# Kernel tuning notes

Hardware: AMD Instinct MI355X
Metric: run time of the kernel (lower is better)

## Reference

```python
import jax, jax.numpy as jnp
import numpy as np

N = 100000
E = 1600000
F_IN = 128
HID = 64
HID2 = 32
NCLS = 2
EPS = 1e-5  # BatchNorm eps


def setup_inputs() -> dict:
    key = jax.random.key(0)
    ks = jax.random.split(key, 12)
    inp = {
        'x': jax.random.normal(ks[0], (N, F_IN), dtype=jnp.float32),
        'edge_index': jax.random.randint(ks[1], (2, E), 0, N, dtype=jnp.int64),
        # GCNConv layer 1: weight [F_IN, HID], bias [HID]
        'W1': jax.random.normal(ks[2], (F_IN, HID), dtype=jnp.float32) / np.sqrt(F_IN),
        'b1': jnp.zeros((HID,), dtype=jnp.float32),
        # GCNConv layer 2
        'W2': jax.random.normal(ks[3], (HID, HID2), dtype=jnp.float32) / np.sqrt(HID),
        'b2': jnp.zeros((HID2,), dtype=jnp.float32),
        # BatchNorm1d params (eval mode: running stats)
        'g1': jax.random.uniform(ks[4], (HID,), dtype=jnp.float32, minval=0.5, maxval=1.5),
        'be1': jax.random.normal(ks[5], (HID,), dtype=jnp.float32) * 0.1,
        'rm1': jax.random.normal(ks[6], (HID,), dtype=jnp.float32) * 0.1,
        'rv1': jax.random.uniform(ks[7], (HID,), dtype=jnp.float32, minval=0.5, maxval=1.5),
        'g2': jax.random.uniform(ks[8], (HID2,), dtype=jnp.float32, minval=0.5, maxval=1.5),
        'be2': jax.random.normal(ks[9], (HID2,), dtype=jnp.float32) * 0.1,
        'rm2': jax.random.normal(ks[10], (HID2,), dtype=jnp.float32) * 0.1,
        'rv2': jax.random.uniform(ks[11], (HID2,), dtype=jnp.float32, minval=0.5, maxval=1.5),
        # classifier
        'Wc': jax.random.normal(jax.random.fold_in(key, 99), (HID2, NCLS), dtype=jnp.float32) / np.sqrt(HID2),
        'bc': jnp.zeros((NCLS,), dtype=jnp.float32),
    }
    return inp


def _gcn_conv(x, src, dst, norm, W, b, n_nodes):
    # PyG GCNConv: transform -> gather source -> norm-weight -> scatter-add -> +bias
    h = x @ W                                  # [N, out]
    msg = h[src] * norm[:, None]               # [E+N, out] gathered messages
    out = jax.ops.segment_sum(msg, dst, num_segments=n_nodes)
    return out + b


def _bn_eval(x, gamma, beta, rmean, rvar):
    return (x - rmean) * (gamma * jax.lax.rsqrt(rvar + EPS)) + beta


def reference(x, edge_index, W1, b1, W2, b2, g1, be1, rm1, rv1, g2, be2, rm2, rv2, Wc, bc):
    n = x.shape[0]
    loop = jnp.arange(n, dtype=edge_index.dtype)
    src = jnp.concatenate([edge_index[0], loop])   # add self-loops
    dst = jnp.concatenate([edge_index[1], loop])
    # symmetric degree normalization on A + I (degree counted at target)
    deg = jax.ops.segment_sum(jnp.ones_like(dst, dtype=x.dtype), dst, num_segments=n)
    dinv = jnp.where(deg > 0, jax.lax.rsqrt(deg), 0.0)
    norm = dinv[src] * dinv[dst]                   # [E+N]

    h = _gcn_conv(x, src, dst, norm, W1, b1, n)
    h = jax.nn.relu(_bn_eval(h, g1, be1, rm1, rv1))
    # dropout: identity in eval mode
    h = _gcn_conv(h, src, dst, norm, W2, b2, n)
    h = jax.nn.relu(_bn_eval(h, g2, be2, rm2, rv2))
    logits = h @ Wc + bc
    return jax.nn.log_softmax(logits, axis=1)
```

## Files before the change

### kernel.cpp

```cpp
#include <hip/hip_runtime.h>
#include <hip/hip_fp16.h>
#include <math.h>

#define F_IN 128
#define HID 64
#define HID2 32
#define EPS_BN 1e-5f
#define BW 128
#define NBMAX 1024
#define CAP 2560
#define CH 8192

__global__ __launch_bounds__(256) void partition_kernel(const int* __restrict__ src, const int* __restrict__ dst,
                                                        int E, int* __restrict__ gcursor,
                                                        unsigned* __restrict__ ebuf) {
    __shared__ int hist[NBMAX];
    __shared__ int start[NBMAX];
    __shared__ int cur[NBMAX];
    __shared__ int gb[NBMAX];
    __shared__ int stmp[256];
    __shared__ unsigned buf[CH];
    int tid = threadIdx.x;
    int e0 = blockIdx.x * CH;
#pragma unroll
    for (int i = 0; i < NBMAX / 256; i++) hist[tid + 256 * i] = 0;
    __syncthreads();
    for (int k = tid; k < CH; k += 256) {
        int e = e0 + k;
        if (e < E) atomicAdd(&hist[dst[e] >> 7], 1);
    }
    __syncthreads();
    int s0 = hist[4 * tid], s1 = hist[4 * tid + 1], s2 = hist[4 * tid + 2], s3 = hist[4 * tid + 3];
    int tsum = s0 + s1 + s2 + s3;
    stmp[tid] = tsum;
    __syncthreads();
    for (int off = 1; off < 256; off <<= 1) {
        int t = (tid >= off) ? stmp[tid - off] : 0;
        __syncthreads();
        stmp[tid] += t;
        __syncthreads();
    }
    int ex = stmp[tid] - tsum;
    start[4 * tid + 0] = ex;                cur[4 * tid + 0] = ex;
    start[4 * tid + 1] = ex + s0;           cur[4 * tid + 1] = ex + s0;
    start[4 * tid + 2] = ex + s0 + s1;      cur[4 * tid + 2] = ex + s0 + s1;
    start[4 * tid + 3] = ex + s0 + s1 + s2; cur[4 * tid + 3] = ex + s0 + s1 + s2;
#pragma unroll
    for (int j = 0; j < 4; j++) {
        int b = 4 * tid + j;
        int h = hist[b];
        gb[b] = h ? atomicAdd(&gcursor[b], h) : 0;
    }
    __syncthreads();
    for (int k = tid; k < CH; k += 256) {
        int e = e0 + k;
        if (e < E) {
            int d = dst[e], s = src[e];
            int p = atomicAdd(&cur[d >> 7], 1);
            buf[p] = ((unsigned)(d & (BW - 1)) << 17) | (unsigned)s;
        }
    }
    __syncthreads();
    int grp = tid >> 2, sub = tid & 3;
    for (int b = grp; b < NBMAX; b += 64) {
        int len = hist[b];
        if (!len) continue;
        int st = start[b];
        unsigned* dp = ebuf + (size_t)b * CAP + gb[b];
        for (int i = sub; i < len; i += 4) dp[i] = buf[st + i];
    }
}

__global__ __launch_bounds__(256) void localsort_kernel(unsigned* __restrict__ ebuf, const int* __restrict__ gcursor,
                                                        int* __restrict__ ns, int* __restrict__ ne,
                                                        float* __restrict__ dinv, int n) {
    __shared__ unsigned lbuf[CAP];
    __shared__ int lhist[BW];
    __shared__ int lcur[BW];
    __shared__ int stmp[256];
    int b = blockIdx.x;
    int tid = threadIdx.x;
    int base = b * CAP;
    int len = gcursor[b];
    int node0 = b * BW;
    int nn = min(BW, n - node0);
    if (tid < BW) lhist[tid] = 0;
    __syncthreads();
    for (int k = tid; k < len; k += 256) {
        unsigned u = ebuf[base + k];
        lbuf[k] = u;
        atomicAdd(&lhist[u >> 17], 1);
    }
    __syncthreads();
    int v = (tid < BW) ? lhist[tid] : 0;
    stmp[tid] = v;
    __syncthreads();
    for (int off = 1; off < 256; off <<= 1) {
        int t = (tid >= off) ? stmp[tid - off] : 0;
        __syncthreads();
        stmp[tid] += t;
        __syncthreads();
    }
    int ex = stmp[tid] - v;
    if (tid < BW) lcur[tid] = ex;
    if (tid < nn) {
        ns[node0 + tid] = base + ex;
        ne[node0 + tid] = base + ex + v;
        dinv[node0 + tid] = rsqrtf((float)(v + 1));
    }
    __syncthreads();
    for (int k = tid; k < len; k += 256) {
        unsigned u = lbuf[k];
        int p = atomicAdd(&lcur[u >> 17], 1);
        ebuf[base + p] = u & 0x1FFFFu;
    }
}

__global__ void constprep_kernel(const float* g1, const float* be1, const float* rm1, const float* rv1, const float* b1,
                                 const float* g2, const float* be2, const float* rm2, const float* rv2, const float* b2,
                                 float* A1, float* B1, float* A2, float* B2) {
    int t = threadIdx.x;
    if (t < HID)  { float s = g1[t] * rsqrtf(rv1[t] + EPS_BN); A1[t] = s; B1[t] = (b1[t] - rm1[t]) * s + be1[t]; }
    if (t < HID2) { float s = g2[t] * rsqrtf(rv2[t] + EPS_BN); A2[t] = s; B2[t] = (b2[t] - rm2[t]) * s + be2[t]; }
}

#define XP1 132
__global__ __launch_bounds__(256) void gemm1_kernel(const float* __restrict__ x, const float* __restrict__ W1,
                                                    const float* __restrict__ dinv, __half* __restrict__ ht1,
                                                    int n) {
    __shared__ float wlds[F_IN * HID];
    __shared__ float xlds[64 * XP1];
    int tid = threadIdx.x;
    {
        const float4* wv = (const float4*)W1;
        float4* wl = (float4*)wlds;
#pragma unroll
        for (int i = 0; i < F_IN * HID / 4 / 256; i++) wl[tid + 256 * i] = wv[tid + 256 * i];
    }
    int row0 = blockIdx.x * 64;
    {
        const float4* xv = (const float4*)(x + (size_t)row0 * F_IN);
        int lim = (n - row0) * (F_IN / 4);
#pragma unroll
        for (int i = 0; i < 8; i++) {
            int f = tid + 256 * i;
            float4 v = make_float4(0.f, 0.f, 0.f, 0.f);
            if (f < lim) v = xv[f];
            int r = f >> 5, kp = (f & 31) * 4;
            *(float4*)&xlds[r * XP1 + kp] = v;
        }
    }
    __syncthreads();
    int col4 = (tid & 15) * 4;
    int rowg = tid >> 4;
    float acc[4][4];
#pragma unroll
    for (int r = 0; r < 4; r++)
#pragma unroll
        for (int c = 0; c < 4; c++) acc[r][c] = 0.f;
#pragma unroll 4
    for (int k = 0; k < F_IN; k += 4) {
        float4 wb[4];
#pragma unroll
        for (int j = 0; j < 4; j++) wb[j] = *(const float4*)&wlds[(k + j) * HID + col4];
#pragma unroll
        for (int r = 0; r < 4; r++) {
            float4 xa = *(const float4*)&xlds[(rowg * 4 + r) * XP1 + k];
            acc[r][0] = fmaf(xa.x, wb[0].x, acc[r][0]); acc[r][1] = fmaf(xa.x, wb[0].y, acc[r][1]);
            acc[r][2] = fmaf(xa.x, wb[0].z, acc[r][2]); acc[r][3] = fmaf(xa.x, wb[0].w, acc[r][3]);
            acc[r][0] = fmaf(xa.y, wb[1].x, acc[r][0]); acc[r][1] = fmaf(xa.y, wb[1].y, acc[r][1]);
            acc[r][2] = fmaf(xa.y, wb[1].z, acc[r][2]); acc[r][3] = fmaf(xa.y, wb[1].w, acc[r][3]);
            acc[r][0] = fmaf(xa.z, wb[2].x, acc[r][0]); acc[r][1] = fmaf(xa.z, wb[2].y, acc[r][1]);
            acc[r][2] = fmaf(xa.z, wb[2].z, acc[r][2]); acc[r][3] = fmaf(xa.z, wb[2].w, acc[r][3]);
            acc[r][0] = fmaf(xa.w, wb[3].x, acc[r][0]); acc[r][1] = fmaf(xa.w, wb[3].y, acc[r][1]);
            acc[r][2] = fmaf(xa.w, wb[3].z, acc[r][2]); acc[r][3] = fmaf(xa.w, wb[3].w, acc[r][3]);
        }
    }
    int rbase = row0 + rowg * 4;
#pragma unroll
    for (int r = 0; r < 4; r++) {
        int row = rbase + r;
        if (row < n) {
            float d = dinv[row];
            __half2 h0, h1;
            h0.x = __float2half(acc[r][0] * d); h0.y = __float2half(acc[r][1] * d);
            h1.x = __float2half(acc[r][2] * d); h1.y = __float2half(acc[r][3] * d);
            __half2* dp = (__half2*)(ht1 + (size_t)row * HID + col4);
            dp[0] = h0; dp[1] = h1;
        }
    }
}

#define XP2 68
__global__ __launch_bounds__(256) void gemm2_kernel(const float* __restrict__ h1p, const float* __restrict__ W2,
                                                    const float* __restrict__ dinv, __half* __restrict__ ht2,
                                                    int n) {
    __shared__ float wlds[HID * HID2];
    __shared__ float xlds[64 * XP2];
    int tid = threadIdx.x;
    {
        const float4* wv = (const float4*)W2;
        float4* wl = (float4*)wlds;
#pragma unroll
        for (int i = 0; i < HID * HID2 / 4 / 256; i++) wl[tid + 256 * i] = wv[tid + 256 * i];
    }
    int row0 = blockIdx.x * 64;
    {
        const float4* xv = (const float4*)(h1p + (size_t)row0 * HID);
        int lim = (n - row0) * (HID / 4);
#pragma unroll
        for (int i = 0; i < 4; i++) {
            int f = tid + 256 * i;
            float4 v = make_float4(0.f, 0.f, 0.f, 0.f);
            if (f < lim) v = xv[f];
            int r = f >> 4, kp = (f & 15) * 4;
            *(float4*)&xlds[r * XP2 + kp] = v;
        }
    }
    __syncthreads();
    int col4 = (tid & 7) * 4;
    int rowg = tid >> 3;
    float acc[2][4];
#pragma unroll
    for (int r = 0; r < 2; r++)
#pragma unroll
        for (int c = 0; c < 4; c++) acc[r][c] = 0.f;
#pragma unroll 4
    for (int k = 0; k < HID; k += 4) {
        float4 wb[4];
#pragma unroll
        for (int j = 0; j < 4; j++) wb[j] = *(const float4*)&wlds[(k + j) * HID2 + col4];
#pragma unroll
        for (int r = 0; r < 2; r++) {
            float4 xa = *(const float4*)&xlds[(rowg * 2 + r) * XP2 + k];
            acc[r][0] = fmaf(xa.x, wb[0].x, acc[r][0]); acc[r][1] = fmaf(xa.x, wb[0].y, acc[r][1]);
            acc[r][2] = fmaf(xa.x, wb[0].z, acc[r][2]); acc[r][3] = fmaf(xa.x, wb[0].w, acc[r][3]);
            acc[r][0] = fmaf(xa.y, wb[1].x, acc[r][0]); acc[r][1] = fmaf(xa.y, wb[1].y, acc[r][1]);
            acc[r][2] = fmaf(xa.y, wb[1].z, acc[r][2]); acc[r][3] = fmaf(xa.y, wb[1].w, acc[r][3]);
            acc[r][0] = fmaf(xa.z, wb[2].x, acc[r][0]); acc[r][1] = fmaf(xa.z, wb[2].y, acc[r][1]);
            acc[r][2] = fmaf(xa.z, wb[2].z, acc[r][2]); acc[r][3] = fmaf(xa.z, wb[2].w, acc[r][3]);
            acc[r][0] = fmaf(xa.w, wb[3].x, acc[r][0]); acc[r][1] = fmaf(xa.w, wb[3].y, acc[r][1]);
            acc[r][2] = fmaf(xa.w, wb[3].z, acc[r][2]); acc[r][3] = fmaf(xa.w, wb[3].w, acc[r][3]);
        }
    }
    int rbase = row0 + rowg * 2;
#pragma unroll
    for (int r = 0; r < 2; r++) {
        int row = rbase + r;
        if (row < n) {
            float d = dinv[row];
            __half2 h0, h1;
            h0.x = __float2half(acc[r][0] * d); h0.y = __float2half(acc[r][1] * d);
            h1.x = __float2half(acc[r][2] * d); h1.y = __float2half(acc[r][3] * d);
            __half2* dp = (__half2*)(ht2 + (size_t)row * HID2 + col4);
            dp[0] = h0; dp[1] = h1;
        }
    }
}

__global__ __launch_bounds__(256) void agg1_kernel(const __half* __restrict__ ht1, const int* __restrict__ ns,
                                                   const int* __restrict__ ne, const int* __restrict__ csr,
                                                   const float* __restrict__ dinv,
                                                   const float* __restrict__ A1, const float* __restrict__ B1,
                                                   float* __restrict__ h1p, int n) {
    int node = (blockIdx.x * blockDim.x + threadIdx.x) >> 6;
    node = __builtin_amdgcn_readfirstlane(node);
    int lane = threadIdx.x & 63;
    if (node >= n) return;
    int s = ns[node], e_end = ne[node];
    float acc = __half2float(ht1[(size_t)node * HID + lane]);
    int e = s;
    for (; e + 8 <= e_end; e += 8) {
        int i0 = csr[e + 0], i1 = csr[e + 1], i2 = csr[e + 2], i3 = csr[e + 3];
        int i4 = csr[e + 4], i5 = csr[e + 5], i6 = csr[e + 6], i7 = csr[e + 7];
        float v0 = __half2float(ht1[(size_t)i0 * HID + lane]);
        float v1 = __half2float(ht1[(size_t)i1 * HID + lane]);
        float v2 = __half2float(ht1[(size_t)i2 * HID + lane]);
        float v3 = __half2float(ht1[(size_t)i3 * HID + lane]);
        float v4 = __half2float(ht1[(size_t)i4 * HID + lane]);
        float v5 = __half2float(ht1[(size_t)i5 * HID + lane]);
        float v6 = __half2float(ht1[(size_t)i6 * HID + lane]);
        float v7 = __half2float(ht1[(size_t)i7 * HID + lane]);
        acc += ((v0 + v1) + (v2 + v3)) + ((v4 + v5) + (v6 + v7));
    }
    for (; e + 4 <= e_end; e += 4) {
        int i0 = csr[e + 0], i1 = csr[e + 1], i2 = csr[e + 2], i3 = csr[e + 3];
        float v0 = __half2float(ht1[(size_t)i0 * HID + lane]);
        float v1 = __half2float(ht1[(size_t)i1 * HID + lane]);
        float v2 = __half2float(ht1[(size_t)i2 * HID + lane]);
        float v3 = __half2float(ht1[(size_t)i3 * HID + lane]);
        acc += (v0 + v1) + (v2 + v3);
    }
    for (; e < e_end; e++) acc += __half2float(ht1[(size_t)csr[e] * HID + lane]);
    float v = acc * dinv[node];
    v = fmaxf(fmaf(v, A1[lane], B1[lane]), 0.f);
    h1p[(size_t)node * HID + lane] = v;
}

__global__ __launch_bounds__(256) void agg2_kernel(const __half* __restrict__ ht2, const int* __restrict__ ns,
                                                   const int* __restrict__ ne, const int* __restrict__ csr,
                                                   const float* __restrict__ dinv,
                                                   const float* __restrict__ A2, const float* __restrict__ B2,
                                                   const float* __restrict__ Wc, const float* __restrict__ bc,
                                                   float* __restrict__ out, int n) {
    int node = (blockIdx.x * blockDim.x + threadIdx.x) >> 6;
    node = __builtin_amdgcn_readfirstlane(node);
    int lane = threadIdx.x & 63;
    if (node >= n) return;
    int c = lane & 31, p = lane >> 5;
    int s = ns[node], e_end = ne[node];
    float acc = (p == 0) ? __half2float(ht2[(size_t)node * HID2 + c]) : 0.f;
    int e = s + p;
    for (; e + 6 < e_end; e += 8) {
        int i0 = csr[e + 0], i1 = csr[e + 2], i2 = csr[e + 4], i3 = csr[e + 6];
        float v0 = __half2float(ht2[(size_t)i0 * HID2 + c]);
        float v1 = __half2float(ht2[(size_t)i1 * HID2 + c]);
        float v2 = __half2float(ht2[(size_t)i2 * HID2 + c]);
        float v3 = __half2float(ht2[(size_t)i3 * HID2 + c]);
        acc += (v0 + v1) + (v2 + v3);
    }
    for (; e < e_end; e += 2) acc += __half2float(ht2[(size_t)csr[e] * HID2 + c]);
    acc += __shfl_xor(acc, 32);
    float v = fmaxf(fmaf(acc * dinv[node], A2[c], B2[c]), 0.f);
    float p0 = v * Wc[c * 2 + 0];
    float p1 = v * Wc[c * 2 + 1];
#pragma unroll
    for (int off = 16; off >= 1; off >>= 1) { p0 += __shfl_xor(p0, off); p1 += __shfl_xor(p1, off); }
    if (lane == 0) {
        float l0 = p0 + bc[0], l1 = p1 + bc[1];
        float m = fmaxf(l0, l1);
        float lse = m + logf(expf(l0 - m) + expf(l1 - m));
        out[(size_t)node * 2 + 0] = l0 - lse;
        out[(size_t)node * 2 + 1] = l1 - lse;
    }
}

extern "C" void kernel_launch(void* const* d_in, const int* in_sizes, int n_in,
                              void* d_out, int out_size, void* d_ws, size_t ws_size,
                              hipStream_t stream) {
    const float* x   = (const float*)d_in[0];
    const int*   ei  = (const int*)d_in[1];
    const float* W1  = (const float*)d_in[2];
    const float* b1  = (const float*)d_in[3];
    const float* W2  = (const float*)d_in[4];
    const float* b2  = (const float*)d_in[5];
    const float* g1  = (const float*)d_in[6];
    const float* be1 = (const float*)d_in[7];
    const float* rm1 = (const float*)d_in[8];
    const float* rv1 = (const float*)d_in[9];
    const float* g2  = (const float*)d_in[10];
    const float* be2 = (const float*)d_in[11];
    const float* rm2 = (const float*)d_in[12];
    const float* rv2 = (const float*)d_in[13];
    const float* Wc  = (const float*)d_in[14];
    const float* bc  = (const float*)d_in[15];
    float* out = (float*)d_out;

    int n = in_sizes[0] / F_IN;
    int E = in_sizes[1] / 2;
    const int* srcv = ei;
    const int* dstv = ei + E;
    int NB = (n + BW - 1) / BW;

    char* ws = (char*)d_ws;
    size_t off = 0;
    auto alloc = [&](size_t bytes) -> char* {
        char* r = ws + off;
        off = (off + bytes + 511) & ~(size_t)511;
        return r;
    };
    int*      gcursor = (int*)alloc((size_t)NB * 4);
    int*      ns      = (int*)alloc((size_t)n * 4);
    int*      ne      = (int*)alloc((size_t)n * 4);
    float*    dinv    = (float*)alloc((size_t)n * 4);
    float*    A1 = (float*)alloc(HID * 4);
    float*    B1 = (float*)alloc(HID * 4);
    float*    A2 = (float*)alloc(HID2 * 4);
    float*    B2 = (float*)alloc(HID2 * 4);
    unsigned* ebuf = (unsigned*)alloc((size_t)NB * CAP * 4);
    __half*   ht1  = (__half*)alloc((size_t)n * HID * 2);
    float*    h1p  = (float*)alloc((size_t)n * HID * 4);
    __half*   ht2  = ht1;

    hipMemsetAsync(gcursor, 0, (size_t)NB * 4, stream);

    int nch = (E + CH - 1) / CH;
    partition_kernel<<<nch, 256, 0, stream>>>(srcv, dstv, E, gcursor, ebuf);
    localsort_kernel<<<NB, 256, 0, stream>>>(ebuf, gcursor, ns, ne, dinv, n);
    constprep_kernel<<<1, 64, 0, stream>>>(g1, be1, rm1, rv1, b1, g2, be2, rm2, rv2, b2, A1, B1, A2, B2);

    int ngb = (n + 63) / 64;
    gemm1_kernel<<<ngb, 256, 0, stream>>>(x, W1, dinv, ht1, n);
    agg1_kernel<<<(n + 3) / 4, 256, 0, stream>>>(ht1, ns, ne, (const int*)ebuf, dinv, A1, B1, h1p, n);
    gemm2_kernel<<<ngb, 256, 0, stream>>>(h1p, W2, dinv, ht2, n);
    agg2_kernel<<<(n + 3) / 4, 256, 0, stream>>>(ht2, ns, ne, (const int*)ebuf, dinv, A2, B2, Wc, bc, out, n);
}
```

Baseline: 310.3 us.

## Replace per-node CSR sort with bucket-level LDS atomic aggregation

Drops the local sort, so edges stay bucketed by 128-node destination block with packed local ids. The aggregation kernels now run one block per bucket and accumulate gathered half-precision features into padded shared-memory tiles with LDS float atomics, then apply BN/ReLU (and the classifier) from shared memory. The partition kernel moves to 1024 threads with one histogram bin per thread, and a small degree kernel replaces localsort for dinv. This removes a full pass over the edge buffer, but float LDS atomics can contend and make summation order nondeterministic, and only NB (~782) blocks run per aggregation.

After: 1.200 ms. 3.87x slower.

```diff
diff --git a/kernel.cpp b/kernel.cpp
--- a/kernel.cpp
+++ b/kernel.cpp
@@ -11,49 +11,42 @@
 #define CAP 2560
 #define CH 8192
 
-__global__ __launch_bounds__(256) void partition_kernel(const int* __restrict__ src, const int* __restrict__ dst,
-                                                        int E, int* __restrict__ gcursor,
-                                                        unsigned* __restrict__ ebuf) {
+__global__ __launch_bounds__(1024) void partition_kernel(const int* __restrict__ src, const int* __restrict__ dst,
+                                                         int E, int* __restrict__ gcursor,
+                                                         unsigned* __restrict__ ebuf) {
     __shared__ int hist[NBMAX];
     __shared__ int start[NBMAX];
     __shared__ int cur[NBMAX];
     __shared__ int gb[NBMAX];
-    __shared__ int stmp[256];
+    __shared__ int sc[1024];
     __shared__ unsigned buf[CH];
     int tid = threadIdx.x;
     int e0 = blockIdx.x * CH;
-#pragma unroll
-    for (int i = 0; i < NBMAX / 256; i++) hist[tid + 256 * i] = 0;
-    __syncthreads();
-    for (int k = tid; k < CH; k += 256) {
-        int e = e0 + k;
+    hist[tid] = 0;
+    __syncthreads();
+#pragma unroll
+    for (int it = 0; it < CH / 1024; it++) {
+        int e = e0 + tid + it * 1024;
         if (e < E) atomicAdd(&hist[dst[e] >> 7], 1);
     }
     __syncthreads();
-    int s0 = hist[4 * tid], s1 = hist[4 * tid + 1], s2 = hist[4 * tid + 2], s3 = hist[4 * tid + 3];
-    int tsum = s0 + s1 + s2 + s3;
-    stmp[tid] = tsum;
-    __syncthreads();
-    for (int off = 1; off < 256; off <<= 1) {
-        int t = (tid >= off) ? stmp[tid - off] : 0;
+    int v = hist[tid];
+    sc[tid] = v;
+    __syncthreads();
+    for (int off = 1; off < 1024; off <<= 1) {
+        int t = (tid >= off) ? sc[tid - off] : 0;
         __syncthreads();
-        stmp[tid] += t;
+        sc[tid] += t;
         __syncthreads();
     }
-    int ex = stmp[tid] - tsum;
-    start[4 * tid + 0] = ex;                cur[4 * tid + 0] = ex;
-    start[4 * tid + 1] = ex + s0;           cur[4 * tid + 1] = ex + s0;
-    start[4 * tid + 2] = ex + s0 + s1;      cur[4 * tid + 2] = ex + s0 + s1;
-    start[4 * tid + 3] = ex + s0 + s1 + s2; cur[4 * tid + 3] = ex + s0 + s1 + s2;
-#pragma unroll
-    for (int j = 0; j < 4; j++) {
-        int b = 4 * tid + j;
-        int h = hist[b];
-        gb[b] = h ? atomicAdd(&gcursor[b], h) : 0;
-    }
-    __syncthreads();
-    for (int k = tid; k < CH; k += 256) {
-        int e = e0 + k;
+    int ex = sc[tid] - v;
+    start[tid] = ex;
+    cur[tid] = ex;
+    gb[tid] = v ? atomicAdd(&gcursor[tid], v) : 0;
+    __syncthreads();
+#pragma unroll
+    for (int it = 0; it < CH / 1024; it++) {
+        int e = e0 + tid + it * 1024;
         if (e < E) {
             int d = dst[e], s = src[e];
             int p = atomicAdd(&cur[d >> 7], 1);
@@ -62,7 +55,7 @@
     }
     __syncthreads();
     int grp = tid >> 2, sub = tid & 3;
-    for (int b = grp; b < NBMAX; b += 64) {
+    for (int b = grp; b < NBMAX; b += 256) {
         int len = hist[b];
         if (!len) continue;
         int st = start[b];
@@ -71,49 +64,18 @@
     }
 }
 
-__global__ __launch_bounds__(256) void localsort_kernel(unsigned* __restrict__ ebuf, const int* __restrict__ gcursor,
-                                                        int* __restrict__ ns, int* __restrict__ ne,
-                                                        float* __restrict__ dinv, int n) {
-    __shared__ unsigned lbuf[CAP];
-    __shared__ int lhist[BW];
-    __shared__ int lcur[BW];
-    __shared__ int stmp[256];
-    int b = blockIdx.x;
-    int tid = threadIdx.x;
-    int base = b * CAP;
-    int len = gcursor[b];
+__global__ __launch_bounds__(256) void degree_kernel(const unsigned* __restrict__ ebuf, const int* __restrict__ gcursor,
+                                                     float* __restrict__ dinv, int n) {
+    __shared__ int ldeg[BW];
+    int b = blockIdx.x, tid = threadIdx.x;
+    int base = b * CAP, len = gcursor[b];
     int node0 = b * BW;
     int nn = min(BW, n - node0);
-    if (tid < BW) lhist[tid] = 0;
-    __syncthreads();
-    for (int k = tid; k < len; k += 256) {
-        unsigned u = ebuf[base + k];
-        lbuf[k] = u;
-        atomicAdd(&lhist[u >> 17], 1);
-    }
-    __syncthreads();
-    int v = (tid < BW) ? lhist[tid] : 0;
-    stmp[tid] = v;
-    __syncthreads();
-    for (int off = 1; off < 256; off <<= 1) {
-        int t = (tid >= off) ? stmp[tid - off] : 0;
-        __syncthreads();
-        stmp[tid] += t;
-        __syncthreads();
-    }
-    int ex = stmp[tid] - v;
-    if (tid < BW) lcur[tid] = ex;
-    if (tid < nn) {
-        ns[node0 + tid] = base + ex;
-        ne[node0 + tid] = base + ex + v;
-        dinv[node0 + tid] = rsqrtf((float)(v + 1));
-    }
-    __syncthreads();
-    for (int k = tid; k < len; k += 256) {
-        unsigned u = lbuf[k];
-        int p = atomicAdd(&lcur[u >> 17], 1);
-        ebuf[base + p] = u & 0x1FFFFu;
-    }
+    if (tid < BW) ldeg[tid] = 0;
+    __syncthreads();
+    for (int k = tid; k < len; k += 256) atomicAdd(&ldeg[ebuf[base + k] >> 17], 1);
+    __syncthreads();
+    if (tid < nn) dinv[node0 + tid] = rsqrtf((float)(ldeg[tid] + 1));
 }
 
 __global__ void constprep_kernel(const float* g1, const float* be1, const float* rm1, const float* rv1, const float* b1,
@@ -258,80 +220,133 @@
     }
 }
 
-__global__ __launch_bounds__(256) void agg1_kernel(const __half* __restrict__ ht1, const int* __restrict__ ns,
-                                                   const int* __restrict__ ne, const int* __restrict__ csr,
-                                                   const float* __restrict__ dinv,
+#define FS1 65
+__global__ __launch_bounds__(256) void agg1_kernel(const __half* __restrict__ ht1, const unsigned* __restrict__ ebuf,
+                                                   const int* __restrict__ gcursor, const float* __restrict__ dinv,
                                                    const float* __restrict__ A1, const float* __restrict__ B1,
                                                    float* __restrict__ h1p, int n) {
-    int node = (blockIdx.x * blockDim.x + threadIdx.x) >> 6;
-    node = __builtin_amdgcn_readfirstlane(node);
-    int lane = threadIdx.x & 63;
-    if (node >= n) return;
-    int s = ns[node], e_end = ne[node];
-    float acc = __half2float(ht1[(size_t)node * HID + lane]);
-    int e = s;
-    for (; e + 8 <= e_end; e += 8) {
-        int i0 = csr[e + 0], i1 = csr[e + 1], i2 = csr[e + 2], i3 = csr[e + 3];
-        int i4 = csr[e + 4], i5 = csr[e + 5], i6 = csr[e + 6], i7 = csr[e + 7];
-        float v0 = __half2float(ht1[(size_t)i0 * HID + lane]);
-        float v1 = __half2float(ht1[(size_t)i1 * HID + lane]);
-        float v2 = __half2float(ht1[(size_t)i2 * HID + lane]);
-        float v3 = __half2float(ht1[(size_t)i3 * HID + lane]);
-        float v4 = __half2float(ht1[(size_t)i4 * HID + lane]);
-        float v5 = __half2float(ht1[(size_t)i5 * HID + lane]);
-        float v6 = __half2float(ht1[(size_t)i6 * HID + lane]);
-        float v7 = __half2float(ht1[(size_t)i7 * HID + lane]);
-        acc += ((v0 + v1) + (v2 + v3)) + ((v4 + v5) + (v6 + v7));
-    }
-    for (; e + 4 <= e_end; e += 4) {
-        int i0 = csr[e + 0], i1 = csr[e + 1], i2 = csr[e + 2], i3 = csr[e + 3];
-        float v0 = __half2float(ht1[(size_t)i0 * HID + lane]);
-        float v1 = __half2float(ht1[(size_t)i1 * HID + lane]);
-        float v2 = __half2float(ht1[(size_t)i2 * HID + lane]);
-        float v3 = __half2float(ht1[(size_t)i3 * HID + lane]);
-        acc += (v0 + v1) + (v2 + v3);
-    }
-    for (; e < e_end; e++) acc += __half2float(ht1[(size_t)csr[e] * HID + lane]);
-    float v = acc * dinv[node];
-    v = fmaxf(fmaf(v, A1[lane], B1[lane]), 0.f);
-    h1p[(size_t)node * HID + lane] = v;
-}
-
-__global__ __launch_bounds__(256) void agg2_kernel(const __half* __restrict__ ht2, const int* __restrict__ ns,
-                                                   const int* __restrict__ ne, const int* __restrict__ csr,
-                                                   const float* __restrict__ dinv,
+    __shared__ float facc[BW * FS1];
+    __shared__ float sA[HID], sB[HID];
+    __shared__ float ldinv[BW];
+    int b = blockIdx.x, tid = threadIdx.x;
+    int base = b * CAP, len = gcursor[b];
+    int node0 = b * BW;
+    int nn = min(BW, n - node0);
+    if (tid < HID) { sA[tid] = A1[tid]; sB[tid] = B1[tid]; }
+    if (tid < nn) ldinv[tid] = dinv[node0 + tid];
+    const __half2* htp = (const __half2*)ht1;
+    for (int idx = tid; idx < nn * 32; idx += 256) {
+        int row = idx >> 5, cp = idx & 31;
+        float2 f = __half22float2(htp[(size_t)(node0 + row) * 32 + cp]);
+        facc[row * FS1 + cp * 2] = f.x;
+        facc[row * FS1 + cp * 2 + 1] = f.y;
+    }
+    __syncthreads();
+    int wid = tid >> 6, lane = tid & 63;
+    int eh = lane >> 5;
+    int cp = lane & 31;
+    int col2 = cp * 2;
+    const unsigned* eb = ebuf + base;
+    int i = wid * 2 + eh;
+    for (; i + 24 < len; i += 32) {
+        unsigned u0 = eb[i], u1 = eb[i + 8], u2 = eb[i + 16], u3 = eb[i + 24];
+        float2 f0 = __half22float2(htp[(size_t)(u0 & 0x1FFFFu) * 32 + cp]);
+        float2 f1 = __half22float2(htp[(size_t)(u1 & 0x1FFFFu) * 32 + cp]);
+        float2 f2 = __half22float2(htp[(size_t)(u2 & 0x1FFFFu) * 32 + cp]);
+        float2 f3 = __half22float2(htp[(size_t)(u3 & 0x1FFFFu) * 32 + cp]);
+        atomicAdd(&facc[(u0 >> 17) * FS1 + col2], f0.x);
+        atomicAdd(&facc[(u0 >> 17) * FS1 + col2 + 1], f0.y);
+        atomicAdd(&facc[(u1 >> 17) * FS1 + col2], f1.x);
+        atomicAdd(&facc[(u1 >> 17) * FS1 + col2 + 1], f1.y);
+        atomicAdd(&facc[(u2 >> 17) * FS1 + col2], f2.x);
+        atomicAdd(&facc[(u2 >> 17) * FS1 + col2 + 1], f2.y);
+        atomicAdd(&facc[(u3 >> 17) * FS1 + col2], f3.x);
+        atomicAdd(&facc[(u3 >> 17) * FS1 + col2 + 1], f3.y);
+    }
+    for (; i < len; i += 8) {
+        unsigned u = eb[i];
+        float2 f = __half22float2(htp[(size_t)(u & 0x1FFFFu) * 32 + cp]);
+        atomicAdd(&facc[(u >> 17) * FS1 + col2], f.x);
+        atomicAdd(&facc[(u >> 17) * FS1 + col2 + 1], f.y);
+    }
+    __syncthreads();
+    for (int idx = tid; idx < nn * 32; idx += 256) {
+        int row = idx >> 5, cc = (idx & 31) * 2;
+        float d = ldinv[row];
+        float2 fr = *(float2*)&facc[row * FS1 + cc];
+        float2 o;
+        o.x = fmaxf(fmaf(fr.x * d, sA[cc], sB[cc]), 0.f);
+        o.y = fmaxf(fmaf(fr.y * d, sA[cc + 1], sB[cc + 1]), 0.f);
+        *(float2*)&h1p[(size_t)(node0 + row) * HID + cc] = o;
+    }
+}
+
+#define FS2 33
+__global__ __launch_bounds__(256) void agg2_kernel(const __half* __restrict__ ht2, const unsigned* __restrict__ ebuf,
+                                                   const int* __restrict__ gcursor, const float* __restrict__ dinv,
                                                    const float* __restrict__ A2, const float* __restrict__ B2,
                                                    const float* __restrict__ Wc, const float* __restrict__ bc,
                                                    float* __restrict__ out, int n) {
-    int node = (blockIdx.x * blockDim.x + threadIdx.x) >> 6;
-    node = __builtin_amdgcn_readfirstlane(node);
-    int lane = threadIdx.x & 63;
-    if (node >= n) return;
-    int c = lane & 31, p = lane >> 5;
-    int s = ns[node], e_end = ne[node];
-    float acc = (p == 0) ? __half2float(ht2[(size_t)node * HID2 + c]) : 0.f;
-    int e = s + p;
-    for (; e + 6 < e_end; e += 8) {
-        int i0 = csr[e + 0], i1 = csr[e + 2], i2 = csr[e + 4], i3 = csr[e + 6];
-        float v0 = __half2float(ht2[(size_t)i0 * HID2 + c]);
-        float v1 = __half2float(ht2[(size_t)i1 * HID2 + c]);
-        float v2 = __half2float(ht2[(size_t)i2 * HID2 + c]);
-        float v3 = __half2float(ht2[(size_t)i3 * HID2 + c]);
-        acc += (v0 + v1) + (v2 + v3);
-    }
-    for (; e < e_end; e += 2) acc += __half2float(ht2[(size_t)csr[e] * HID2 + c]);
-    acc += __shfl_xor(acc, 32);
-    float v = fmaxf(fmaf(acc * dinv[node], A2[c], B2[c]), 0.f);
-    float p0 = v * Wc[c * 2 + 0];
-    float p1 = v * Wc[c * 2 + 1];
-#pragma unroll
-    for (int off = 16; off >= 1; off >>= 1) { p0 += __shfl_xor(p0, off); p1 += __shfl_xor(p1, off); }
-    if (lane == 0) {
+    __shared__ float facc[BW * FS2];
+    __shared__ float sA[HID2], sB[HID2], sW[HID2 * 2];
+    __shared__ float ldinv[BW];
+    int b = blockIdx.x, tid = threadIdx.x;
+    int base = b * CAP, len = gcursor[b];
+    int node0 = b * BW;
+    int nn = min(BW, n - node0);
+    if (tid < HID2) { sA[tid] = A2[tid]; sB[tid] = B2[tid]; }
+    if (tid >= 64 && tid < 64 + HID2 * 2) sW[tid - 64] = Wc[tid - 64];
+    if (tid < nn) ldinv[tid] = dinv[node0 + tid];
+    const __half2* htp = (const __half2*)ht2;
+    for (int idx = tid; idx < nn * 16; idx += 256) {
+        int row = idx >> 4, cp = idx & 15;
+        float2 f = __half22float2(htp[(size_t)(node0 + row) * 16 + cp]);
+        facc[row * FS2 + cp * 2] = f.x;
+        facc[row * FS2 + cp * 2 + 1] = f.y;
+    }
+    __syncthreads();
+    int wid = tid >> 6, lane = tid & 63;
+    int eq = lane >> 4;
+    int cp = lane & 15;
+    int col2 = cp * 2;
+    const unsigned* eb = ebuf + base;
+    int i = wid * 4 + eq;
+    for (; i + 48 < len; i += 64) {
+        unsigned u0 = eb[i], u1 = eb[i + 16], u2 = eb[i + 32], u3 = eb[i + 48];
+        float2 f0 = __half22float2(htp[(size_t)(u0 & 0x1FFFFu) * 16 + cp]);
+        float2 f1 = __half22float2(htp[(size_t)(u1 & 0x1FFFFu) * 16 + cp]);
+        float2 f2 = __half22float2(htp[(size_t)(u2 & 0x1FFFFu) * 16 + cp]);
+        float2 f3 = __half22float2(htp[(size_t)(u3 & 0x1FFFFu) * 16 + cp]);
+        atomicAdd(&facc[(u0 >> 17) * FS2 + col2], f0.x);
+        atomicAdd(&facc[(u0 >> 17) * FS2 + col2 + 1], f0.y);
+        atomicAdd(&facc[(u1 >> 17) * FS2 + col2], f1.x);
+        atomicAdd(&facc[(u1 >> 17) * FS2 + col2 + 1], f1.y);
+        atomicAdd(&facc[(u2 >> 17) * FS2 + col2], f2.x);
+        atomicAdd(&facc[(u2 >> 17) * FS2 + col2 + 1], f2.y);
+        atomicAdd(&facc[(u3 >> 17) * FS2 + col2], f3.x);
+        atomicAdd(&facc[(u3 >> 17) * FS2 + col2 + 1], f3.y);
+    }
+    for (; i < len; i += 16) {
+        unsigned u = eb[i];
+        float2 f = __half22float2(htp[(size_t)(u & 0x1FFFFu) * 16 + cp]);
+        atomicAdd(&facc[(u >> 17) * FS2 + col2], f.x);
+        atomicAdd(&facc[(u >> 17) * FS2 + col2 + 1], f.y);
+    }
+    __syncthreads();
+    if (tid < nn) {
+        float d = ldinv[tid];
+        float p0 = 0.f, p1 = 0.f;
+#pragma unroll
+        for (int c = 0; c < HID2; c++) {
+            float v = fmaxf(fmaf(facc[tid * FS2 + c] * d, sA[c], sB[c]), 0.f);
+            p0 = fmaf(v, sW[c * 2 + 0], p0);
+            p1 = fmaf(v, sW[c * 2 + 1], p1);
+        }
         float l0 = p0 + bc[0], l1 = p1 + bc[1];
         float m = fmaxf(l0, l1);
         float lse = m + logf(expf(l0 - m) + expf(l1 - m));
-        out[(size_t)node * 2 + 0] = l0 - lse;
-        out[(size_t)node * 2 + 1] = l1 - lse;
+        float2 o; o.x = l0 - lse; o.y = l1 - lse;
+        *(float2*)&out[(size_t)(node0 + tid) * 2] = o;
     }
 }
 
@@ -370,8 +385,6 @@
         return r;
     };
     int*      gcursor = (int*)alloc((size_t)NB * 4);
-    int*      ns      = (int*)alloc((size_t)n * 4);
-    int*      ne      = (int*)alloc((size_t)n * 4);
     float*    dinv    = (float*)alloc((size_t)n * 4);
     float*    A1 = (float*)alloc(HID * 4);
     float*    B1 = (float*)alloc(HID * 4);
@@ -385,13 +398,13 @@
     hipMemsetAsync(gcursor, 0, (size_t)NB * 4, stream);
 
     int nch = (E + CH - 1) / CH;
-    partition_kernel<<<nch, 256, 0, stream>>>(srcv, dstv, E, gcursor, ebuf);
-    localsort_kernel<<<NB, 256, 0, stream>>>(ebuf, gcursor, ns, ne, dinv, n);
+    partition_kernel<<<nch, 1024, 0, stream>>>(srcv, dstv, E, gcursor, ebuf);
+    degree_kernel<<<NB, 256, 0, stream>>>(ebuf, gcursor, dinv, n);
     constprep_kernel<<<1, 64, 0, stream>>>(g1, be1, rm1, rv1, b1, g2, be2, rm2, rv2, b2, A1, B1, A2, B2);
 
     int ngb = (n + 63) / 64;
     gemm1_kernel<<<ngb, 256, 0, stream>>>(x, W1, dinv, ht1, n);
-    agg1_kernel<<<(n + 3) / 4, 256, 0, stream>>>(ht1, ns, ne, (const int*)ebuf, dinv, A1, B1, h1p, n);
+    agg1_kernel<<<NB, 256, 0, stream>>>(ht1, ebuf, gcursor, dinv, A1, B1, h1p, n);
     gemm2_kernel<<<ngb, 256, 0, stream>>>(h1p, W2, dinv, ht2, n);
-    agg2_kernel<<<(n + 3) / 4, 256, 0, stream>>>(ht2, ns, ne, (const int*)ebuf, dinv, A2, B2, Wc, bc, out, n);
-}
+    agg2_kernel<<<NB, 256, 0, stream>>>(ht2, ebuf, gcursor, dinv, A2, B2, Wc, bc, out, n);
+}
```

## Widen partition blocks and split neighbor lists across half-wave groups in aggregation

Applied to the files above, without the earlier changes.

The partition kernel now runs 1024 threads per block, one histogram bin per thread, with a single-bin scan and a wider copy-out loop. Both aggregation kernels now read features as half2, so 32 (agg1) or 16 (agg2) lanes cover a row. The remaining lanes split the neighbor list into 2 or 4 interleaved edge streams, which are combined with cross-lane shuffles. This is meant to raise memory-level parallelism and use wider loads in the gather-bound aggregation. The cost is extra shuffles and a longer 1024-wide scan with more barriers in partition.

Result: faster. 301.3 us (-2.9%).

```diff
diff --git a/kernel.cpp b/kernel.cpp
--- a/kernel.cpp
+++ b/kernel.cpp
@@ -11,49 +11,42 @@
 #define CAP 2560
 #define CH 8192
 
-__global__ __launch_bounds__(256) void partition_kernel(const int* __restrict__ src, const int* __restrict__ dst,
-                                                        int E, int* __restrict__ gcursor,
-                                                        unsigned* __restrict__ ebuf) {
+__global__ __launch_bounds__(1024) void partition_kernel(const int* __restrict__ src, const int* __restrict__ dst,
+                                                         int E, int* __restrict__ gcursor,
+                                                         unsigned* __restrict__ ebuf) {
     __shared__ int hist[NBMAX];
     __shared__ int start[NBMAX];
     __shared__ int cur[NBMAX];
     __shared__ int gb[NBMAX];
-    __shared__ int stmp[256];
+    __shared__ int sc[1024];
     __shared__ unsigned buf[CH];
     int tid = threadIdx.x;
     int e0 = blockIdx.x * CH;
-#pragma unroll
-    for (int i = 0; i < NBMAX / 256; i++) hist[tid + 256 * i] = 0;
-    __syncthreads();
-    for (int k = tid; k < CH; k += 256) {
-        int e = e0 + k;
+    hist[tid] = 0;
+    __syncthreads();
+#pragma unroll
+    for (int it = 0; it < CH / 1024; it++) {
+        int e = e0 + tid + it * 1024;
         if (e < E) atomicAdd(&hist[dst[e] >> 7], 1);
     }
     __syncthreads();
-    int s0 = hist[4 * tid], s1 = hist[4 * tid + 1], s2 = hist[4 * tid + 2], s3 = hist[4 * tid + 3];
-    int tsum = s0 + s1 + s2 + s3;
-    stmp[tid] = tsum;
-    __syncthreads();
-    for (int off = 1; off < 256; off <<= 1) {
-        int t = (tid >= off) ? stmp[tid - off] : 0;
+    int v = hist[tid];
+    sc[tid] = v;
+    __syncthreads();
+    for (int off = 1; off < 1024; off <<= 1) {
+        int t = (tid >= off) ? sc[tid - off] : 0;
         __syncthreads();
-        stmp[tid] += t;
+        sc[tid] += t;
         __syncthreads();
     }
-    int ex = stmp[tid] - tsum;
-    start[4 * tid + 0] = ex;                cur[4 * tid + 0] = ex;
-    start[4 * tid + 1] = ex + s0;           cur[4 * tid + 1] = ex + s0;
-    start[4 * tid + 2] = ex + s0 + s1;      cur[4 * tid + 2] = ex + s0 + s1;
-    start[4 * tid + 3] = ex + s0 + s1 + s2; cur[4 * tid + 3] = ex + s0 + s1 + s2;
-#pragma unroll
-    for (int j = 0; j < 4; j++) {
-        int b = 4 * tid + j;
-        int h = hist[b];
-        gb[b] = h ? atomicAdd(&gcursor[b], h) : 0;
-    }
-    __syncthreads();
-    for (int k = tid; k < CH; k += 256) {
-        int e = e0 + k;
+    int ex = sc[tid] - v;
+    start[tid] = ex;
+    cur[tid] = ex;
+    gb[tid] = v ? atomicAdd(&gcursor[tid], v) : 0;
+    __syncthreads();
+#pragma unroll
+    for (int it = 0; it < CH / 1024; it++) {
+        int e = e0 + tid + it * 1024;
         if (e < E) {
             int d = dst[e], s = src[e];
             int p = atomicAdd(&cur[d >> 7], 1);
@@ -62,7 +55,7 @@
     }
     __syncthreads();
     int grp = tid >> 2, sub = tid & 3;
-    for (int b = grp; b < NBMAX; b += 64) {
+    for (int b = grp; b < NBMAX; b += 256) {
         int len = hist[b];
         if (!len) continue;
         int st = start[b];
@@ -264,37 +257,45 @@
                                                    const float* __restrict__ A1, const float* __restrict__ B1,
                                                    float* __restrict__ h1p, int n) {
     int node = (blockIdx.x * blockDim.x + threadIdx.x) >> 6;
-    node = __builtin_amdgcn_readfirstlane(node);
+    if (node >= n) return;
     int lane = threadIdx.x & 63;
-    if (node >= n) return;
+    int eh = lane >> 5, cp = lane & 31;
+    const __half2* htp = (const __half2*)ht1;
     int s = ns[node], e_end = ne[node];
-    float acc = __half2float(ht1[(size_t)node * HID + lane]);
-    int e = s;
-    for (; e + 8 <= e_end; e += 8) {
-        int i0 = csr[e + 0], i1 = csr[e + 1], i2 = csr[e + 2], i3 = csr[e + 3];
-        int i4 = csr[e + 4], i5 = csr[e + 5], i6 = csr[e + 6], i7 = csr[e + 7];
-        float v0 = __half2float(ht1[(size_t)i0 * HID + lane]);
-        float v1 = __half2float(ht1[(size_t)i1 * HID + lane]);
-        float v2 = __half2float(ht1[(size_t)i2 * HID + lane]);
-        float v3 = __half2float(ht1[(size_t)i3 * HID + lane]);
-        float v4 = __half2float(ht1[(size_t)i4 * HID + lane]);
-        float v5 = __half2float(ht1[(size_t)i5 * HID + lane]);
-        float v6 = __half2float(ht1[(size_t)i6 * HID + lane]);
-        float v7 = __half2float(ht1[(size_t)i7 * HID + lane]);
-        acc += ((v0 + v1) + (v2 + v3)) + ((v4 + v5) + (v6 + v7));
-    }
-    for (; e + 4 <= e_end; e += 4) {
-        int i0 = csr[e + 0], i1 = csr[e + 1], i2 = csr[e + 2], i3 = csr[e + 3];
-        float v0 = __half2float(ht1[(size_t)i0 * HID + lane]);
-        float v1 = __half2float(ht1[(size_t)i1 * HID + lane]);
-        float v2 = __half2float(ht1[(size_t)i2 * HID + lane]);
-        float v3 = __half2float(ht1[(size_t)i3 * HID + lane]);
-        acc += (v0 + v1) + (v2 + v3);
-    }
-    for (; e < e_end; e++) acc += __half2float(ht1[(size_t)csr[e] * HID + lane]);
-    float v = acc * dinv[node];
-    v = fmaxf(fmaf(v, A1[lane], B1[lane]), 0.f);
-    h1p[(size_t)node * HID + lane] = v;
+    float ax = 0.f, ay = 0.f;
+    if (eh == 0) {
+        float2 f = __half22float2(htp[(size_t)node * 32 + cp]);
+        ax = f.x; ay = f.y;
+    }
+    int i = s + eh;
+    for (; i + 14 < e_end; i += 16) {
+        int i0 = csr[i + 0], i1 = csr[i + 2], i2 = csr[i + 4], i3 = csr[i + 6];
+        int i4 = csr[i + 8], i5 = csr[i + 10], i6 = csr[i + 12], i7 = csr[i + 14];
+        float2 f0 = __half22float2(htp[(size_t)i0 * 32 + cp]);
+        float2 f1 = __half22float2(htp[(size_t)i1 * 32 + cp]);
+        float2 f2 = __half22float2(htp[(size_t)i2 * 32 + cp]);
+        float2 f3 = __half22float2(htp[(size_t)i3 * 32 + cp]);
+        float2 f4 = __half22float2(htp[(size_t)i4 * 32 + cp]);
+        float2 f5 = __half22float2(htp[(size_t)i5 * 32 + cp]);
+        float2 f6 = __half22float2(htp[(size_t)i6 * 32 + cp]);
+        float2 f7 = __half22float2(htp[(size_t)i7 * 32 + cp]);
+        ax += ((f0.x + f1.x) + (f2.x + f3.x)) + ((f4.x + f5.x) + (f6.x + f7.x));
+        ay += ((f0.y + f1.y) + (f2.y + f3.y)) + ((f4.y + f5.y) + (f6.y + f7.y));
+    }
+    for (; i < e_end; i += 2) {
+        float2 f = __half22float2(htp[(size_t)csr[i] * 32 + cp]);
+        ax += f.x; ay += f.y;
+    }
+    ax += __shfl_xor(ax, 32);
+    ay += __shfl_xor(ay, 32);
+    if (eh == 0) {
+        float d = dinv[node];
+        int c0 = cp * 2;
+        float2 o;
+        o.x = fmaxf(fmaf(ax * d, A1[c0], B1[c0]), 0.f);
+        o.y = fmaxf(fmaf(ay * d, A1[c0 + 1], B1[c0 + 1]), 0.f);
+        *(float2*)&h1p[(size_t)node * HID + c0] = o;
+    }
 }
 
 __global__ __launch_bounds__(256) void agg2_kernel(const __half* __restrict__ ht2, const int* __restrict__ ns,
@@ -304,34 +305,46 @@
                                                    const float* __restrict__ Wc, const float* __restrict__ bc,
                                                    float* __restrict__ out, int n) {
     int node = (blockIdx.x * blockDim.x + threadIdx.x) >> 6;
-    node = __builtin_amdgcn_readfirstlane(node);
+    if (node >= n) return;
     int lane = threadIdx.x & 63;
-    if (node >= n) return;
-    int c = lane & 31, p = lane >> 5;
+    int eq = lane >> 4, cp = lane & 15;
+    const __half2* htp = (const __half2*)ht2;
     int s = ns[node], e_end = ne[node];
-    float acc = (p == 0) ? __half2float(ht2[(size_t)node * HID2 + c]) : 0.f;
-    int e = s + p;
-    for (; e + 6 < e_end; e += 8) {
-        int i0 = csr[e + 0], i1 = csr[e + 2], i2 = csr[e + 4], i3 = csr[e + 6];
-        float v0 = __half2float(ht2[(size_t)i0 * HID2 + c]);
-        float v1 = __half2float(ht2[(size_t)i1 * HID2 + c]);
-        float v2 = __half2float(ht2[(size_t)i2 * HID2 + c]);
-        float v3 = __half2float(ht2[(size_t)i3 * HID2 + c]);
-        acc += (v0 + v1) + (v2 + v3);
-    }
-    for (; e < e_end; e += 2) acc += __half2float(ht2[(size_t)csr[e] * HID2 + c]);
-    acc += __shfl_xor(acc, 32);
-    float v = fmaxf(fmaf(acc * dinv[node], A2[c], B2[c]), 0.f);
-    float p0 = v * Wc[c * 2 + 0];
-    float p1 = v * Wc[c * 2 + 1];
-#pragma unroll
-    for (int off = 16; off >= 1; off >>= 1) { p0 += __shfl_xor(p0, off); p1 += __shfl_xor(p1, off); }
+    float ax = 0.f, ay = 0.f;
+    if (eq == 0) {
+        float2 f = __half22float2(htp[(size_t)node * 16 + cp]);
+        ax = f.x; ay = f.y;
+    }
+    int i = s + eq;
+    for (; i + 12 < e_end; i += 16) {
+        int i0 = csr[i + 0], i1 = csr[i + 4], i2 = csr[i + 8], i3 = csr[i + 12];
+        float2 f0 = __half22float2(htp[(size_t)i0 * 16 + cp]);
+        float2 f1 = __half22float2(htp[(size_t)i1 * 16 + cp]);
+        float2 f2 = __half22float2(htp[(size_t)i2 * 16 + cp]);
+        float2 f3 = __half22float2(htp[(size_t)i3 * 16 + cp]);
+        ax += (f0.x + f1.x) + (f2.x + f3.x);
+        ay += (f0.y + f1.y) + (f2.y + f3.y);
+    }
+    for (; i < e_end; i += 4) {
+        float2 f = __half22float2(htp[(size_t)csr[i] * 16 + cp]);
+        ax += f.x; ay += f.y;
+    }
+    ax += __shfl_xor(ax, 32); ay += __shfl_xor(ay, 32);
+    ax += __shfl_xor(ax, 16); ay += __shfl_xor(ay, 16);
+    float d = dinv[node];
+    int c0 = cp * 2;
+    float v0 = fmaxf(fmaf(ax * d, A2[c0], B2[c0]), 0.f);
+    float v1 = fmaxf(fmaf(ay * d, A2[c0 + 1], B2[c0 + 1]), 0.f);
+    float p0 = v0 * Wc[c0 * 2 + 0] + v1 * Wc[c0 * 2 + 2];
+    float p1 = v0 * Wc[c0 * 2 + 1] + v1 * Wc[c0 * 2 + 3];
+#pragma unroll
+    for (int off = 8; off >= 1; off >>= 1) { p0 += __shfl_xor(p0, off); p1 += __shfl_xor(p1, off); }
     if (lane == 0) {
         float l0 = p0 + bc[0], l1 = p1 + bc[1];
         float m = fmaxf(l0, l1);
         float lse = m + logf(expf(l0 - m) + expf(l1 - m));
-        out[(size_t)node * 2 + 0] = l0 - lse;
-        out[(size_t)node * 2 + 1] = l1 - lse;
+        float2 o; o.x = l0 - lse; o.y = l1 - lse;
+        *(float2*)&out[(size_t)node * 2] = o;
     }
 }
 
@@ -385,7 +398,7 @@
     hipMemsetAsync(gcursor, 0, (size_t)NB * 4, stream);
 
     int nch = (E + CH - 1) / CH;
-    partition_kernel<<<nch, 256, 0, stream>>>(srcv, dstv, E, gcursor, ebuf);
+    partition_kernel<<<nch, 1024, 0, stream>>>(srcv, dstv, E, gcursor, ebuf);
     localsort_kernel<<<NB, 256, 0, stream>>>(ebuf, gcursor, ns, ne, dinv, n);
     constprep_kernel<<<1, 64, 0, stream>>>(g1, be1, rm1, rv1, b1, g2, be2, rm2, rv2, b2, A1, B1, A2, B2);
 
```
